# Optimization experiments

Measured on AMD Instinct MI355X. Metric: run time of the kernel, lower is better.

## Reference

```python
import jax, jax.numpy as jnp
import numpy as np

NUM_EXPERTS = 64
TOP_K = 2
AUX_COEF = 0.001
Z_COEF = 0.001


def setup_inputs() -> dict:
    key = jax.random.key(0)
    k1, k2 = jax.random.split(key)
    hidden_states = jax.random.normal(k1, (16384, 4096), dtype=jnp.float32)
    W_gate = jax.random.normal(k2, (NUM_EXPERTS, 4096), dtype=jnp.float32) * 0.02
    return {"hidden_states": hidden_states, "W_gate": W_gate}


def reference(hidden_states, W_gate):
    # Gate GEMM: [N, H] x [E, H]^T -> [N, E]
    router_logits = jnp.einsum('nh,eh->ne', hidden_states, W_gate)
    router_probs = jax.nn.softmax(router_logits, axis=-1)

    # Top-k selection + renormalization
    expert_weights, expert_indices = jax.lax.top_k(router_probs, TOP_K)
    expert_weights = expert_weights / jnp.sum(expert_weights, axis=-1, keepdims=True)

    # Load-balancing loss: num_experts * sum_i f_i * P_i
    num_tokens = router_probs.shape[0]
    one_hot = jax.nn.one_hot(expert_indices, NUM_EXPERTS, dtype=jnp.float32)  # [N, K, E]
    tokens_per_expert = one_hot.sum(axis=(0, 1))  # [E]
    f = tokens_per_expert / (num_tokens * TOP_K)
    P = router_probs.mean(axis=0)
    lb_loss = NUM_EXPERTS * jnp.sum(f * P)

    # Z-loss: mean of logsumexp(logits)^2
    log_z = jax.nn.logsumexp(router_logits, axis=-1)
    z_loss = jnp.mean(log_z ** 2)

    aux_loss = AUX_COEF * lb_loss + Z_COEF * z_loss
    return expert_weights, expert_indices, aux_loss
```

## Files before the change

### kernel.cpp

```cpp
#include <hip/hip_runtime.h>
#include <hip/hip_bf16.h>

#define NTOK 16384
#define HD   4096
#define NE   64
#define TTILE 32
#define NBLK (NTOK / TTILE)

typedef __bf16 bf16x8 __attribute__((ext_vector_type(8)));
typedef __bf16 bf16x4 __attribute__((ext_vector_type(4)));
typedef float  f32x4  __attribute__((ext_vector_type(4)));

__device__ __forceinline__ f32x4 mfma16(bf16x8 a, bf16x8 b, f32x4 c) {
    return __builtin_amdgcn_mfma_f32_16x16x32_bf16(a, b, c, 0, 0, 0);
}

#define SAB 40
#define SL  68

__device__ __forceinline__ void cvt_split(float4 v, bf16x4& hi, bf16x4& lo) {
    float x[4] = {v.x, v.y, v.z, v.w};
    #pragma unroll
    for (int e = 0; e < 4; ++e) {
        __bf16 h = (__bf16)x[e];
        hi[e] = h;
        lo[e] = (__bf16)(x[e] - (float)h);
    }
}

__global__ void zero_ws_kernel(float* ws) {
    int i = threadIdx.x;
    if (i < 129) ws[i] = 0.0f;
}

__global__ __launch_bounds__(256) void router_kernel(
    const float* __restrict__ hs,
    const float* __restrict__ Wg,
    float* __restrict__ out,
    float* __restrict__ ws)
{
    __shared__ __bf16 sAhi[2][TTILE * SAB];
    __shared__ __bf16 sAlo[2][TTILE * SAB];
    __shared__ __bf16 sBhi[2][NE * SAB];
    __shared__ __bf16 sBlo[2][NE * SAB];
    __shared__ float  sLog[TTILE * SL];
    __shared__ float  sInv[TTILE];
    __shared__ float  sPp[4 * 64];
    __shared__ float  sCnt[64];
    __shared__ float  sZ;

    const int tid = threadIdx.x;
    const int t0  = blockIdx.x * TTILE;

    if (tid < 64) sCnt[tid] = 0.0f;
    if (tid == 0) sZ = 0.0f;

    const int r1 = tid >> 3;
    const int c4 = (tid & 7) * 4;
    const float* gA = hs + (size_t)(t0 + r1) * HD + c4;
    const float* gB = Wg + (size_t)r1 * HD + c4;
    const int oA  = r1 * SAB + c4;
    const int oB1 = r1 * SAB + c4;
    const int oB2 = (r1 + 32) * SAB + c4;

    const int lane = tid & 63;
    const int wv   = tid >> 6;
    const int wr   = (wv >> 1) * 16;
    const int wc   = (wv & 1) * 32;
    const int fm   = lane & 15;
    const int fq   = lane >> 4;
    const int fk   = fq * 8;

    f32x4 acc[2];
    acc[0] = (f32x4){0.f, 0.f, 0.f, 0.f};
    acc[1] = (f32x4){0.f, 0.f, 0.f, 0.f};

    {
        float4 a0 = *(const float4*)(gA);
        float4 b0 = *(const float4*)(gB);
        float4 b1 = *(const float4*)(gB + 32 * HD);
        bf16x4 h, l;
        cvt_split(a0, h, l); *(bf16x4*)&sAhi[0][oA]  = h; *(bf16x4*)&sAlo[0][oA]  = l;
        cvt_split(b0, h, l); *(bf16x4*)&sBhi[0][oB1] = h; *(bf16x4*)&sBlo[0][oB1] = l;
        cvt_split(b1, h, l); *(bf16x4*)&sBhi[0][oB2] = h; *(bf16x4*)&sBlo[0][oB2] = l;
    }
    __syncthreads();

    const int NIT = HD / 32;
    for (int it = 0; it < NIT; ++it) {
        const int cur = it & 1;
        const bool more = (it + 1) < NIT;
        float4 na0, nb0, nb1;
        if (more) {
            const int k0 = (it + 1) * 32;
            na0 = *(const float4*)(gA + k0);
            nb0 = *(const float4*)(gB + k0);
            nb1 = *(const float4*)(gB + 32 * HD + k0);
        }

        bf16x8 ahi, alo, bhi[2], blo[2];
        {
            const int aoff = (wr + fm) * SAB + fk;
            ahi = *(const bf16x8*)&sAhi[cur][aoff];
            alo = *(const bf16x8*)&sAlo[cur][aoff];
        }
        #pragma unroll
        for (int j = 0; j < 2; ++j) {
            const int boff = (wc + j * 16 + fm) * SAB + fk;
            bhi[j] = *(const bf16x8*)&sBhi[cur][boff];
            blo[j] = *(const bf16x8*)&sBlo[cur][boff];
        }
        #pragma unroll
        for (int j = 0; j < 2; ++j) {
            acc[j] = mfma16(ahi, bhi[j], acc[j]);
            acc[j] = mfma16(ahi, blo[j], acc[j]);
            acc[j] = mfma16(alo, bhi[j], acc[j]);
            acc[j] = mfma16(alo, blo[j], acc[j]);
        }

        if (more) {
            const int nb = cur ^ 1;
            bf16x4 h, l;
            cvt_split(na0, h, l); *(bf16x4*)&sAhi[nb][oA]  = h; *(bf16x4*)&sAlo[nb][oA]  = l;
            cvt_split(nb0, h, l); *(bf16x4*)&sBhi[nb][oB1] = h; *(bf16x4*)&sBlo[nb][oB1] = l;
            cvt_split(nb1, h, l); *(bf16x4*)&sBhi[nb][oB2] = h; *(bf16x4*)&sBlo[nb][oB2] = l;
        }
        __syncthreads();
    }

    #pragma unroll
    for (int j = 0; j < 2; ++j)
        #pragma unroll
        for (int r = 0; r < 4; ++r) {
            const int tokl = wr + fq * 4 + r;
            const int expl = wc + j * 16 + fm;
            sLog[tokl * SL + expl] = acc[j][r];
        }
    __syncthreads();

    const int g = tid >> 3;
    const int l = tid & 7;
    float* Lrow = &sLog[g * SL + l * 8];
    float lv[8];
    float m = -3.0e38f;
    #pragma unroll
    for (int c = 0; c < 8; ++c) { lv[c] = Lrow[c]; m = fmaxf(m, lv[c]); }
    m = fmaxf(m, __shfl_xor(m, 1, 64));
    m = fmaxf(m, __shfl_xor(m, 2, 64));
    m = fmaxf(m, __shfl_xor(m, 4, 64));

    float v1 = -3.0e38f, v2 = -3.0e38f; int i1 = 0, i2 = 0;
    float ssum = 0.0f;
    #pragma unroll
    for (int c = 0; c < 8; ++c) {
        const float val = lv[c]; const int idx = l * 8 + c;
        const float ev = __expf(val - m);
        Lrow[c] = ev;
        ssum += ev;
        if (val > v1) { v2 = v1; i2 = i1; v1 = val; i1 = idx; }
        else if (val > v2) { v2 = val; i2 = idx; }
    }
    ssum += __shfl_xor(ssum, 1, 64);
    ssum += __shfl_xor(ssum, 2, 64);
    ssum += __shfl_xor(ssum, 4, 64);

    #pragma unroll
    for (int s = 1; s <= 4; s <<= 1) {
        const float ov1 = __shfl_xor(v1, s, 64);
        const int   oi1 = __shfl_xor(i1, s, 64);
        const float ov2 = __shfl_xor(v2, s, 64);
        const int   oi2 = __shfl_xor(i2, s, 64);
        float n1, n2; int ni1, ni2;
        const bool ofirst = (ov1 > v1) || (ov1 == v1 && oi1 < i1);
        if (ofirst) {
            n1 = ov1; ni1 = oi1;
            const bool osec = (ov2 > v1) || (ov2 == v1 && oi2 < i1);
            n2 = osec ? ov2 : v1; ni2 = osec ? oi2 : i1;
        } else {
            n1 = v1; ni1 = i1;
            const bool asec = (v2 > ov1) || (v2 == ov1 && i2 < oi1);
            n2 = asec ? v2 : ov1; ni2 = asec ? i2 : oi1;
        }
        v1 = n1; i1 = ni1; v2 = n2; i2 = ni2;
    }

    if (l == 0) {
        const float e1 = __expf(v1 - m), e2 = __expf(v2 - m);
        const float winv = 1.0f / (e1 + e2);
        const int token = t0 + g;
        out[2 * token]     = e1 * winv;
        out[2 * token + 1] = e2 * winv;
        out[2 * NTOK + 2 * token]     = (float)i1;
        out[2 * NTOK + 2 * token + 1] = (float)i2;
        const float lse = m + __logf(ssum);
        atomicAdd(&sZ, lse * lse);
        atomicAdd(&sCnt[i1], 1.0f);
        atomicAdd(&sCnt[i2], 1.0f);
        sInv[g] = 1.0f / ssum;
    }
    __syncthreads();

    {
        const int e = tid & 63;
        const int q = tid >> 6;
        float part = 0.0f;
        #pragma unroll
        for (int t = 0; t < 8; ++t) {
            const int tok = q * 8 + t;
            part += sLog[tok * SL + e] * sInv[tok];
        }
        sPp[q * 64 + e] = part;
    }
    __syncthreads();
    if (tid < 64) {
        const float ps = sPp[tid] + sPp[64 + tid] + sPp[128 + tid] + sPp[192 + tid];
        atomicAdd(&ws[tid], ps);
        atomicAdd(&ws[64 + tid], sCnt[tid]);
    }
    if (tid == 0) atomicAdd(&ws[128], sZ);
}

__global__ void finalize_kernel(const float* __restrict__ ws, float* __restrict__ out) {
    const int e = threadIdx.x;
    const float P = ws[e] * (1.0f / NTOK);
    const float f = ws[64 + e] * (1.0f / (NTOK * 2));
    float term = f * P;
    #pragma unroll
    for (int s = 32; s >= 1; s >>= 1) term += __shfl_xor(term, s, 64);
    if (e == 0) {
        const float lb = 64.0f * term;
        const float z  = ws[128] * (1.0f / NTOK);
        out[4 * NTOK] = 0.001f * lb + 0.001f * z;
    }
}

extern "C" void kernel_launch(void* const* d_in, const int* in_sizes, int n_in,
                              void* d_out, int out_size, void* d_ws, size_t ws_size,
                              hipStream_t stream) {
    const float* hs = (const float*)d_in[0];
    const float* Wg = (const float*)d_in[1];
    float* out = (float*)d_out;
    float* ws  = (float*)d_ws;

    hipLaunchKernelGGL(zero_ws_kernel, dim3(1), dim3(256), 0, stream, ws);
    hipLaunchKernelGGL(router_kernel, dim3(NBLK), dim3(256), 0, stream, hs, Wg, out, ws);
    hipLaunchKernelGGL(finalize_kernel, dim3(1), dim3(64), 0, stream, ws, out);
}
```

Before: 398.6 us.

## Pre-split gate weights into bf16 hi/lo and load MFMA fragments directly from global

Adds a prep kernel that converts W_gate once per call into bf16 hi/lo arrays in workspace (also zeroing the accumulators), and rewrites the router main loop to drop the LDS double-buffer and barriers, loading A and B fragments straight from global memory into registers, with a one-step register prefetch of A. This removes per-block redundant conversion of the weight matrix, LDS traffic and __syncthreads each k-step. In exchange every wave re-reads B from L2 and A loads are narrower, per-lane strided accesses, so memory latency is now hidden only by occupancy and the single prefetch. A fallback path with per-block on-the-fly conversion runs if the workspace is too small.

```diff
diff --git a/kernel.cpp b/kernel.cpp
--- a/kernel.cpp
+++ b/kernel.cpp
@@ -6,6 +6,12 @@
 #define NE   64
 #define TTILE 32
 #define NBLK (NTOK / TTILE)
+#define NIT  (HD / 32)
+
+#define SL  68
+
+#define WS_ACC_FLOATS 192
+#define B_ELEMS (NE * HD)
 
 typedef __bf16 bf16x8 __attribute__((ext_vector_type(8)));
 typedef __bf16 bf16x4 __attribute__((ext_vector_type(4)));
@@ -14,9 +20,6 @@
 __device__ __forceinline__ f32x4 mfma16(bf16x8 a, bf16x8 b, f32x4 c) {
     return __builtin_amdgcn_mfma_f32_16x16x32_bf16(a, b, c, 0, 0, 0);
 }
-
-#define SAB 40
-#define SL  68
 
 __device__ __forceinline__ void cvt_split(float4 v, bf16x4& hi, bf16x4& lo) {
     float x[4] = {v.x, v.y, v.z, v.w};
@@ -33,35 +36,45 @@
     if (i < 129) ws[i] = 0.0f;
 }
 
+__global__ __launch_bounds__(256) void prep_kernel(
+    const float* __restrict__ Wg, float* __restrict__ ws)
+{
+    const int tid = threadIdx.x;
+    if (blockIdx.x == 0 && tid < 129) ws[tid] = 0.0f;
+    __bf16* Bhi = (__bf16*)(ws + WS_ACC_FLOATS);
+    __bf16* Blo = Bhi + B_ELEMS;
+    const int i = (blockIdx.x * 256 + tid) * 8;
+    float4 v0 = *(const float4*)(Wg + i);
+    float4 v1 = *(const float4*)(Wg + i + 4);
+    bf16x4 h0, l0, h1, l1;
+    cvt_split(v0, h0, l0);
+    cvt_split(v1, h1, l1);
+    *(bf16x4*)(Bhi + i)     = h0;
+    *(bf16x4*)(Bhi + i + 4) = h1;
+    *(bf16x4*)(Blo + i)     = l0;
+    *(bf16x4*)(Blo + i + 4) = l1;
+}
+
+template<bool PRE>
 __global__ __launch_bounds__(256) void router_kernel(
     const float* __restrict__ hs,
     const float* __restrict__ Wg,
+    const __bf16* __restrict__ Bhi,
+    const __bf16* __restrict__ Blo,
     float* __restrict__ out,
     float* __restrict__ ws)
 {
-    __shared__ __bf16 sAhi[2][TTILE * SAB];
-    __shared__ __bf16 sAlo[2][TTILE * SAB];
-    __shared__ __bf16 sBhi[2][NE * SAB];
-    __shared__ __bf16 sBlo[2][NE * SAB];
-    __shared__ float  sLog[TTILE * SL];
-    __shared__ float  sInv[TTILE];
-    __shared__ float  sPp[4 * 64];
-    __shared__ float  sCnt[64];
-    __shared__ float  sZ;
+    __shared__ float sLog[TTILE * SL];
+    __shared__ float sInv[TTILE];
+    __shared__ float sPp[4 * 64];
+    __shared__ float sCnt[64];
+    __shared__ float sZ;
 
     const int tid = threadIdx.x;
     const int t0  = blockIdx.x * TTILE;
 
     if (tid < 64) sCnt[tid] = 0.0f;
     if (tid == 0) sZ = 0.0f;
-
-    const int r1 = tid >> 3;
-    const int c4 = (tid & 7) * 4;
-    const float* gA = hs + (size_t)(t0 + r1) * HD + c4;
-    const float* gB = Wg + (size_t)r1 * HD + c4;
-    const int oA  = r1 * SAB + c4;
-    const int oB1 = r1 * SAB + c4;
-    const int oB2 = (r1 + 32) * SAB + c4;
 
     const int lane = tid & 63;
     const int wv   = tid >> 6;
@@ -71,62 +84,80 @@
     const int fq   = lane >> 4;
     const int fk   = fq * 8;
 
+    const float* pA = hs + (size_t)(t0 + wr + fm) * HD + fk;
+
+    const __bf16* pBh = nullptr;
+    const __bf16* pBl = nullptr;
+    const float*  pBf = nullptr;
+    if constexpr (PRE) {
+        pBh = Bhi + (size_t)(wc + fm) * HD + fk;
+        pBl = Blo + (size_t)(wc + fm) * HD + fk;
+    } else {
+        pBf = Wg + (size_t)(wc + fm) * HD + fk;
+    }
+
     f32x4 acc[2];
     acc[0] = (f32x4){0.f, 0.f, 0.f, 0.f};
     acc[1] = (f32x4){0.f, 0.f, 0.f, 0.f};
 
-    {
-        float4 a0 = *(const float4*)(gA);
-        float4 b0 = *(const float4*)(gB);
-        float4 b1 = *(const float4*)(gB + 32 * HD);
-        bf16x4 h, l;
-        cvt_split(a0, h, l); *(bf16x4*)&sAhi[0][oA]  = h; *(bf16x4*)&sAlo[0][oA]  = l;
-        cvt_split(b0, h, l); *(bf16x4*)&sBhi[0][oB1] = h; *(bf16x4*)&sBlo[0][oB1] = l;
-        cvt_split(b1, h, l); *(bf16x4*)&sBhi[0][oB2] = h; *(bf16x4*)&sBlo[0][oB2] = l;
-    }
-    __syncthreads();
-
-    const int NIT = HD / 32;
-    for (int it = 0; it < NIT; ++it) {
-        const int cur = it & 1;
-        const bool more = (it + 1) < NIT;
-        float4 na0, nb0, nb1;
-        if (more) {
-            const int k0 = (it + 1) * 32;
-            na0 = *(const float4*)(gA + k0);
-            nb0 = *(const float4*)(gB + k0);
-            nb1 = *(const float4*)(gB + 32 * HD + k0);
-        }
-
-        bf16x8 ahi, alo, bhi[2], blo[2];
+    auto step = [&](float4 ca0, float4 ca1) {
+        bf16x8 bh0, bl0, bh1, bl1;
+        if constexpr (PRE) {
+            bh0 = *(const bf16x8*)(pBh);
+            bh1 = *(const bf16x8*)(pBh + 16 * HD);
+            bl0 = *(const bf16x8*)(pBl);
+            bl1 = *(const bf16x8*)(pBl + 16 * HD);
+            pBh += 32; pBl += 32;
+        } else {
+            float4 f00 = *(const float4*)(pBf);
+            float4 f01 = *(const float4*)(pBf + 4);
+            float4 f10 = *(const float4*)(pBf + 16 * HD);
+            float4 f11 = *(const float4*)(pBf + 16 * HD + 4);
+            pBf += 32;
+            bf16x4 h, l;
+            cvt_split(f00, h, l);
+            #pragma unroll
+            for (int e = 0; e < 4; ++e) { bh0[e] = h[e]; bl0[e] = l[e]; }
+            cvt_split(f01, h, l);
+            #pragma unroll
+            for (int e = 0; e < 4; ++e) { bh0[4+e] = h[e]; bl0[4+e] = l[e]; }
+            cvt_split(f10, h, l);
+            #pragma unroll
+            for (int e = 0; e < 4; ++e) { bh1[e] = h[e]; bl1[e] = l[e]; }
+            cvt_split(f11, h, l);
+            #pragma unroll
+            for (int e = 0; e < 4; ++e) { bh1[4+e] = h[e]; bl1[4+e] = l[e]; }
+        }
+        bf16x8 ahi, alo;
         {
-            const int aoff = (wr + fm) * SAB + fk;
-            ahi = *(const bf16x8*)&sAhi[cur][aoff];
-            alo = *(const bf16x8*)&sAlo[cur][aoff];
-        }
-        #pragma unroll
-        for (int j = 0; j < 2; ++j) {
-            const int boff = (wc + j * 16 + fm) * SAB + fk;
-            bhi[j] = *(const bf16x8*)&sBhi[cur][boff];
-            blo[j] = *(const bf16x8*)&sBlo[cur][boff];
-        }
-        #pragma unroll
-        for (int j = 0; j < 2; ++j) {
-            acc[j] = mfma16(ahi, bhi[j], acc[j]);
-            acc[j] = mfma16(ahi, blo[j], acc[j]);
-            acc[j] = mfma16(alo, bhi[j], acc[j]);
-            acc[j] = mfma16(alo, blo[j], acc[j]);
-        }
-
-        if (more) {
-            const int nb = cur ^ 1;
             bf16x4 h, l;
-            cvt_split(na0, h, l); *(bf16x4*)&sAhi[nb][oA]  = h; *(bf16x4*)&sAlo[nb][oA]  = l;
-            cvt_split(nb0, h, l); *(bf16x4*)&sBhi[nb][oB1] = h; *(bf16x4*)&sBlo[nb][oB1] = l;
-            cvt_split(nb1, h, l); *(bf16x4*)&sBhi[nb][oB2] = h; *(bf16x4*)&sBlo[nb][oB2] = l;
-        }
-        __syncthreads();
-    }
+            cvt_split(ca0, h, l);
+            #pragma unroll
+            for (int e = 0; e < 4; ++e) { ahi[e] = h[e]; alo[e] = l[e]; }
+            cvt_split(ca1, h, l);
+            #pragma unroll
+            for (int e = 0; e < 4; ++e) { ahi[4+e] = h[e]; alo[4+e] = l[e]; }
+        }
+        acc[0] = mfma16(ahi, bh0, acc[0]);
+        acc[0] = mfma16(ahi, bl0, acc[0]);
+        acc[0] = mfma16(alo, bh0, acc[0]);
+        acc[0] = mfma16(alo, bl0, acc[0]);
+        acc[1] = mfma16(ahi, bh1, acc[1]);
+        acc[1] = mfma16(ahi, bl1, acc[1]);
+        acc[1] = mfma16(alo, bh1, acc[1]);
+        acc[1] = mfma16(alo, bl1, acc[1]);
+    };
+
+    float4 a0 = *(const float4*)(pA);
+    float4 a1 = *(const float4*)(pA + 4);
+    for (int it = 0; it < NIT - 1; ++it) {
+        float4 n0 = *(const float4*)(pA + 32);
+        float4 n1 = *(const float4*)(pA + 36);
+        pA += 32;
+        step(a0, a1);
+        a0 = n0; a1 = n1;
+    }
+    step(a0, a1);
 
     #pragma unroll
     for (int j = 0; j < 2; ++j)
@@ -242,7 +273,18 @@
     float* out = (float*)d_out;
     float* ws  = (float*)d_ws;
 
-    hipLaunchKernelGGL(zero_ws_kernel, dim3(1), dim3(256), 0, stream, ws);
-    hipLaunchKernelGGL(router_kernel, dim3(NBLK), dim3(256), 0, stream, hs, Wg, out, ws);
+    const size_t need = (size_t)WS_ACC_FLOATS * sizeof(float)
+                      + (size_t)B_ELEMS * 2 * sizeof(__bf16);
+    if (ws_size >= need) {
+        const __bf16* Bhi = (const __bf16*)(ws + WS_ACC_FLOATS);
+        const __bf16* Blo = Bhi + B_ELEMS;
+        hipLaunchKernelGGL(prep_kernel, dim3(128), dim3(256), 0, stream, Wg, ws);
+        hipLaunchKernelGGL((router_kernel<true>), dim3(NBLK), dim3(256), 0, stream,
+                           hs, Wg, Bhi, Blo, out, ws);
+    } else {
+        hipLaunchKernelGGL(zero_ws_kernel, dim3(1), dim3(256), 0, stream, ws);
+        hipLaunchKernelGGL((router_kernel<false>), dim3(NBLK), dim3(256), 0, stream,
+                           hs, Wg, (const __bf16*)nullptr, (const __bf16*)nullptr, out, ws);
+    }
     hipLaunchKernelGGL(finalize_kernel, dim3(1), dim3(64), 0, stream, ws, out);
 }
```

Result: slower. 478.8 us (+20.1%).

## Pre-split gate weights to bf16 hi/lo once and stream B fragments directly into registers

Applied to the files above, without the earlier changes.

A prep kernel converts W_gate into bf16 hi/lo arrays in workspace once per call, merged with workspace zeroing. The main kernel then loads B fragments straight from global (L2-resident) into registers instead of each block re-reading fp32 W, splitting it and staging it through LDS. This removes redundant per-block conversion work and B shared-memory traffic, at the cost of an extra launch and more global/L2 loads per wave. A fallback path keeps the old kernel if the workspace is too small.

```diff
diff --git a/kernel.cpp b/kernel.cpp
--- a/kernel.cpp
+++ b/kernel.cpp
@@ -6,6 +6,13 @@
 #define NE   64
 #define TTILE 32
 #define NBLK (NTOK / TTILE)
+#define NIT  (HD / 32)
+
+#define SAB 40
+#define SL  68
+
+#define WS_ACC_FLOATS 192
+#define B_ELEMS (NE * HD)
 
 typedef __bf16 bf16x8 __attribute__((ext_vector_type(8)));
 typedef __bf16 bf16x4 __attribute__((ext_vector_type(4)));
@@ -14,9 +21,6 @@
 __device__ __forceinline__ f32x4 mfma16(bf16x8 a, bf16x8 b, f32x4 c) {
     return __builtin_amdgcn_mfma_f32_16x16x32_bf16(a, b, c, 0, 0, 0);
 }
-
-#define SAB 40
-#define SL  68
 
 __device__ __forceinline__ void cvt_split(float4 v, bf16x4& hi, bf16x4& lo) {
     float x[4] = {v.x, v.y, v.z, v.w};
@@ -33,16 +37,34 @@
     if (i < 129) ws[i] = 0.0f;
 }
 
-__global__ __launch_bounds__(256) void router_kernel(
+__global__ __launch_bounds__(256) void prep_kernel(
+    const float* __restrict__ Wg, float* __restrict__ ws)
+{
+    const int tid = threadIdx.x;
+    if (blockIdx.x == 0 && tid < 129) ws[tid] = 0.0f;
+    __bf16* Bhi = (__bf16*)(ws + WS_ACC_FLOATS);
+    __bf16* Blo = Bhi + B_ELEMS;
+    const int i = (blockIdx.x * 256 + tid) * 8;
+    float4 v0 = *(const float4*)(Wg + i);
+    float4 v1 = *(const float4*)(Wg + i + 4);
+    bf16x4 h0, l0, h1, l1;
+    cvt_split(v0, h0, l0);
+    cvt_split(v1, h1, l1);
+    *(bf16x4*)(Bhi + i)     = h0;
+    *(bf16x4*)(Bhi + i + 4) = h1;
+    *(bf16x4*)(Blo + i)     = l0;
+    *(bf16x4*)(Blo + i + 4) = l1;
+}
+
+__global__ __launch_bounds__(256) void router_pre_kernel(
     const float* __restrict__ hs,
-    const float* __restrict__ Wg,
+    const __bf16* __restrict__ Bhi,
+    const __bf16* __restrict__ Blo,
     float* __restrict__ out,
     float* __restrict__ ws)
 {
     __shared__ __bf16 sAhi[2][TTILE * SAB];
     __shared__ __bf16 sAlo[2][TTILE * SAB];
-    __shared__ __bf16 sBhi[2][NE * SAB];
-    __shared__ __bf16 sBlo[2][NE * SAB];
     __shared__ float  sLog[TTILE * SL];
     __shared__ float  sInv[TTILE];
     __shared__ float  sPp[4 * 64];
@@ -58,10 +80,7 @@
     const int r1 = tid >> 3;
     const int c4 = (tid & 7) * 4;
     const float* gA = hs + (size_t)(t0 + r1) * HD + c4;
-    const float* gB = Wg + (size_t)r1 * HD + c4;
-    const int oA  = r1 * SAB + c4;
-    const int oB1 = r1 * SAB + c4;
-    const int oB2 = (r1 + 32) * SAB + c4;
+    const int oA = r1 * SAB + c4;
 
     const int lane = tid & 63;
     const int wv   = tid >> 6;
@@ -71,59 +90,65 @@
     const int fq   = lane >> 4;
     const int fk   = fq * 8;
 
+    const __bf16* gBh = Bhi + (size_t)(wc + fm) * HD + fk;
+    const __bf16* gBl = Blo + (size_t)(wc + fm) * HD + fk;
+
     f32x4 acc[2];
     acc[0] = (f32x4){0.f, 0.f, 0.f, 0.f};
     acc[1] = (f32x4){0.f, 0.f, 0.f, 0.f};
 
     {
         float4 a0 = *(const float4*)(gA);
-        float4 b0 = *(const float4*)(gB);
-        float4 b1 = *(const float4*)(gB + 32 * HD);
         bf16x4 h, l;
-        cvt_split(a0, h, l); *(bf16x4*)&sAhi[0][oA]  = h; *(bf16x4*)&sAlo[0][oA]  = l;
-        cvt_split(b0, h, l); *(bf16x4*)&sBhi[0][oB1] = h; *(bf16x4*)&sBlo[0][oB1] = l;
-        cvt_split(b1, h, l); *(bf16x4*)&sBhi[0][oB2] = h; *(bf16x4*)&sBlo[0][oB2] = l;
-    }
-    __syncthreads();
-
-    const int NIT = HD / 32;
+        cvt_split(a0, h, l);
+        *(bf16x4*)&sAhi[0][oA] = h;
+        *(bf16x4*)&sAlo[0][oA] = l;
+    }
+    bf16x8 cbh[2], cbl[2];
+    cbh[0] = *(const bf16x8*)(gBh);
+    cbh[1] = *(const bf16x8*)(gBh + 16 * HD);
+    cbl[0] = *(const bf16x8*)(gBl);
+    cbl[1] = *(const bf16x8*)(gBl + 16 * HD);
+    __syncthreads();
+
+    #pragma unroll 2
     for (int it = 0; it < NIT; ++it) {
         const int cur = it & 1;
         const bool more = (it + 1) < NIT;
-        float4 na0, nb0, nb1;
+
+        float4 na;
+        bf16x8 nbh0, nbh1, nbl0, nbl1;
         if (more) {
             const int k0 = (it + 1) * 32;
-            na0 = *(const float4*)(gA + k0);
-            nb0 = *(const float4*)(gB + k0);
-            nb1 = *(const float4*)(gB + 32 * HD + k0);
-        }
-
-        bf16x8 ahi, alo, bhi[2], blo[2];
+            na   = *(const float4*)(gA + k0);
+            nbh0 = *(const bf16x8*)(gBh + k0);
+            nbh1 = *(const bf16x8*)(gBh + 16 * HD + k0);
+            nbl0 = *(const bf16x8*)(gBl + k0);
+            nbl1 = *(const bf16x8*)(gBl + 16 * HD + k0);
+        }
+
+        bf16x8 ahi, alo;
         {
             const int aoff = (wr + fm) * SAB + fk;
             ahi = *(const bf16x8*)&sAhi[cur][aoff];
             alo = *(const bf16x8*)&sAlo[cur][aoff];
         }
-        #pragma unroll
-        for (int j = 0; j < 2; ++j) {
-            const int boff = (wc + j * 16 + fm) * SAB + fk;
-            bhi[j] = *(const bf16x8*)&sBhi[cur][boff];
-            blo[j] = *(const bf16x8*)&sBlo[cur][boff];
-        }
-        #pragma unroll
-        for (int j = 0; j < 2; ++j) {
-            acc[j] = mfma16(ahi, bhi[j], acc[j]);
-            acc[j] = mfma16(ahi, blo[j], acc[j]);
-            acc[j] = mfma16(alo, bhi[j], acc[j]);
-            acc[j] = mfma16(alo, blo[j], acc[j]);
-        }
+        acc[0] = mfma16(ahi, cbh[0], acc[0]);
+        acc[0] = mfma16(ahi, cbl[0], acc[0]);
+        acc[0] = mfma16(alo, cbh[0], acc[0]);
+        acc[0] = mfma16(alo, cbl[0], acc[0]);
+        acc[1] = mfma16(ahi, cbh[1], acc[1]);
+        acc[1] = mfma16(ahi, cbl[1], acc[1]);
+        acc[1] = mfma16(alo, cbh[1], acc[1]);
+        acc[1] = mfma16(alo, cbl[1], acc[1]);
 
         if (more) {
-            const int nb = cur ^ 1;
             bf16x4 h, l;
-            cvt_split(na0, h, l); *(bf16x4*)&sAhi[nb][oA]  = h; *(bf16x4*)&sAlo[nb][oA]  = l;
-            cvt_split(nb0, h, l); *(bf16x4*)&sBhi[nb][oB1] = h; *(bf16x4*)&sBlo[nb][oB1] = l;
-            cvt_split(nb1, h, l); *(bf16x4*)&sBhi[nb][oB2] = h; *(bf16x4*)&sBlo[nb][oB2] = l;
+            cvt_split(na, h, l);
+            *(bf16x4*)&sAhi[cur ^ 1][oA] = h;
+            *(bf16x4*)&sAlo[cur ^ 1][oA] = l;
+            cbh[0] = nbh0; cbh[1] = nbh1;
+            cbl[0] = nbl0; cbl[1] = nbl1;
         }
         __syncthreads();
     }
@@ -220,6 +245,192 @@
     if (tid == 0) atomicAdd(&ws[128], sZ);
 }
 
+__global__ __launch_bounds__(256) void router_fb_kernel(
+    const float* __restrict__ hs,
+    const float* __restrict__ Wg,
+    float* __restrict__ out,
+    float* __restrict__ ws)
+{
+    __shared__ __bf16 sAhi[2][TTILE * SAB];
+    __shared__ __bf16 sAlo[2][TTILE * SAB];
+    __shared__ __bf16 sBhi[2][NE * SAB];
+    __shared__ __bf16 sBlo[2][NE * SAB];
+    __shared__ float  sLog[TTILE * SL];
+    __shared__ float  sInv[TTILE];
+    __shared__ float  sPp[4 * 64];
+    __shared__ float  sCnt[64];
+    __shared__ float  sZ;
+
+    const int tid = threadIdx.x;
+    const int t0  = blockIdx.x * TTILE;
+
+    if (tid < 64) sCnt[tid] = 0.0f;
+    if (tid == 0) sZ = 0.0f;
+
+    const int r1 = tid >> 3;
+    const int c4 = (tid & 7) * 4;
+    const float* gA = hs + (size_t)(t0 + r1) * HD + c4;
+    const float* gB = Wg + (size_t)r1 * HD + c4;
+    const int oA  = r1 * SAB + c4;
+    const int oB1 = r1 * SAB + c4;
+    const int oB2 = (r1 + 32) * SAB + c4;
+
+    const int lane = tid & 63;
+    const int wv   = tid >> 6;
+    const int wr   = (wv >> 1) * 16;
+    const int wc   = (wv & 1) * 32;
+    const int fm   = lane & 15;
+    const int fq   = lane >> 4;
+    const int fk   = fq * 8;
+
+    f32x4 acc[2];
+    acc[0] = (f32x4){0.f, 0.f, 0.f, 0.f};
+    acc[1] = (f32x4){0.f, 0.f, 0.f, 0.f};
+
+    {
+        float4 a0 = *(const float4*)(gA);
+        float4 b0 = *(const float4*)(gB);
+        float4 b1 = *(const float4*)(gB + 32 * HD);
+        bf16x4 h, l;
+        cvt_split(a0, h, l); *(bf16x4*)&sAhi[0][oA]  = h; *(bf16x4*)&sAlo[0][oA]  = l;
+        cvt_split(b0, h, l); *(bf16x4*)&sBhi[0][oB1] = h; *(bf16x4*)&sBlo[0][oB1] = l;
+        cvt_split(b1, h, l); *(bf16x4*)&sBhi[0][oB2] = h; *(bf16x4*)&sBlo[0][oB2] = l;
+    }
+    __syncthreads();
+
+    for (int it = 0; it < NIT; ++it) {
+        const int cur = it & 1;
+        const bool more = (it + 1) < NIT;
+        float4 na0, nb0, nb1;
+        if (more) {
+            const int k0 = (it + 1) * 32;
+            na0 = *(const float4*)(gA + k0);
+            nb0 = *(const float4*)(gB + k0);
+            nb1 = *(const float4*)(gB + 32 * HD + k0);
+        }
+
+        bf16x8 ahi, alo, bhi[2], blo[2];
+        {
+            const int aoff = (wr + fm) * SAB + fk;
+            ahi = *(const bf16x8*)&sAhi[cur][aoff];
+            alo = *(const bf16x8*)&sAlo[cur][aoff];
+        }
+        #pragma unroll
+        for (int j = 0; j < 2; ++j) {
+            const int boff = (wc + j * 16 + fm) * SAB + fk;
+            bhi[j] = *(const bf16x8*)&sBhi[cur][boff];
+            blo[j] = *(const bf16x8*)&sBlo[cur][boff];
+        }
+        #pragma unroll
+        for (int j = 0; j < 2; ++j) {
+            acc[j] = mfma16(ahi, bhi[j], acc[j]);
+            acc[j] = mfma16(ahi, blo[j], acc[j]);
+            acc[j] = mfma16(alo, bhi[j], acc[j]);
+            acc[j] = mfma16(alo, blo[j], acc[j]);
+        }
+
+        if (more) {
+            const int nb = cur ^ 1;
+            bf16x4 h, l;
+            cvt_split(na0, h, l); *(bf16x4*)&sAhi[nb][oA]  = h; *(bf16x4*)&sAlo[nb][oA]  = l;
+            cvt_split(nb0, h, l); *(bf16x4*)&sBhi[nb][oB1] = h; *(bf16x4*)&sBlo[nb][oB1] = l;
+            cvt_split(nb1, h, l); *(bf16x4*)&sBhi[nb][oB2] = h; *(bf16x4*)&sBlo[nb][oB2] = l;
+        }
+        __syncthreads();
+    }
+
+    #pragma unroll
+    for (int j = 0; j < 2; ++j)
+        #pragma unroll
+        for (int r = 0; r < 4; ++r) {
+            const int tokl = wr + fq * 4 + r;
+            const int expl = wc + j * 16 + fm;
+            sLog[tokl * SL + expl] = acc[j][r];
+        }
+    __syncthreads();
+
+    const int g = tid >> 3;
+    const int l = tid & 7;
+    float* Lrow = &sLog[g * SL + l * 8];
+    float lv[8];
+    float m = -3.0e38f;
+    #pragma unroll
+    for (int c = 0; c < 8; ++c) { lv[c] = Lrow[c]; m = fmaxf(m, lv[c]); }
+    m = fmaxf(m, __shfl_xor(m, 1, 64));
+    m = fmaxf(m, __shfl_xor(m, 2, 64));
+    m = fmaxf(m, __shfl_xor(m, 4, 64));
+
+    float v1 = -3.0e38f, v2 = -3.0e38f; int i1 = 0, i2 = 0;
+    float ssum = 0.0f;
+    #pragma unroll
+    for (int c = 0; c < 8; ++c) {
+        const float val = lv[c]; const int idx = l * 8 + c;
+        const float ev = __expf(val - m);
+        Lrow[c] = ev;
+        ssum += ev;
+        if (val > v1) { v2 = v1; i2 = i1; v1 = val; i1 = idx; }
+        else if (val > v2) { v2 = val; i2 = idx; }
+    }
+    ssum += __shfl_xor(ssum, 1, 64);
+    ssum += __shfl_xor(ssum, 2, 64);
+    ssum += __shfl_xor(ssum, 4, 64);
+
+    #pragma unroll
+    for (int s = 1; s <= 4; s <<= 1) {
+        const float ov1 = __shfl_xor(v1, s, 64);
+        const int   oi1 = __shfl_xor(i1, s, 64);
+        const float ov2 = __shfl_xor(v2, s, 64);
+        const int   oi2 = __shfl_xor(i2, s, 64);
+        float n1, n2; int ni1, ni2;
+        const bool ofirst = (ov1 > v1) || (ov1 == v1 && oi1 < i1);
+        if (ofirst) {
+            n1 = ov1; ni1 = oi1;
+            const bool osec = (ov2 > v1) || (ov2 == v1 && oi2 < i1);
+            n2 = osec ? ov2 : v1; ni2 = osec ? oi2 : i1;
+        } else {
+            n1 = v1; ni1 = i1;
+            const bool asec = (v2 > ov1) || (v2 == ov1 && i2 < oi1);
+            n2 = asec ? v2 : ov1; ni2 = asec ? i2 : oi1;
+        }
+        v1 = n1; i1 = ni1; v2 = n2; i2 = ni2;
+    }
+
+    if (l == 0) {
+        const float e1 = __expf(v1 - m), e2 = __expf(v2 - m);
+        const float winv = 1.0f / (e1 + e2);
+        const int token = t0 + g;
+        out[2 * token]     = e1 * winv;
+        out[2 * token + 1] = e2 * winv;
+        out[2 * NTOK + 2 * token]     = (float)i1;
+        out[2 * NTOK + 2 * token + 1] = (float)i2;
+        const float lse = m + __logf(ssum);
+        atomicAdd(&sZ, lse * lse);
+        atomicAdd(&sCnt[i1], 1.0f);
+        atomicAdd(&sCnt[i2], 1.0f);
+        sInv[g] = 1.0f / ssum;
+    }
+    __syncthreads();
+
+    {
+        const int e = tid & 63;
+        const int q = tid >> 6;
+        float part = 0.0f;
+        #pragma unroll
+        for (int t = 0; t < 8; ++t) {
+            const int tok = q * 8 + t;
+            part += sLog[tok * SL + e] * sInv[tok];
+        }
+        sPp[q * 64 + e] = part;
+    }
+    __syncthreads();
+    if (tid < 64) {
+        const float ps = sPp[tid] + sPp[64 + tid] + sPp[128 + tid] + sPp[192 + tid];
+        atomicAdd(&ws[tid], ps);
+        atomicAdd(&ws[64 + tid], sCnt[tid]);
+    }
+    if (tid == 0) atomicAdd(&ws[128], sZ);
+}
+
 __global__ void finalize_kernel(const float* __restrict__ ws, float* __restrict__ out) {
     const int e = threadIdx.x;
     const float P = ws[e] * (1.0f / NTOK);
@@ -242,7 +453,18 @@
     float* out = (float*)d_out;
     float* ws  = (float*)d_ws;
 
-    hipLaunchKernelGGL(zero_ws_kernel, dim3(1), dim3(256), 0, stream, ws);
-    hipLaunchKernelGGL(router_kernel, dim3(NBLK), dim3(256), 0, stream, hs, Wg, out, ws);
+    const size_t need = (size_t)WS_ACC_FLOATS * sizeof(float)
+                      + (size_t)B_ELEMS * 2 * sizeof(__bf16);
+    if (ws_size >= need) {
+        const __bf16* Bhi = (const __bf16*)(ws + WS_ACC_FLOATS);
+        const __bf16* Blo = Bhi + B_ELEMS;
+        hipLaunchKernelGGL(prep_kernel, dim3(128), dim3(256), 0, stream, Wg, ws);
+        hipLaunchKernelGGL(router_pre_kernel, dim3(NBLK), dim3(256), 0, stream,
+                           hs, Bhi, Blo, out, ws);
+    } else {
+        hipLaunchKernelGGL(zero_ws_kernel, dim3(1), dim3(256), 0, stream, ws);
+        hipLaunchKernelGGL(router_fb_kernel, dim3(NBLK), dim3(256), 0, stream,
+                           hs, Wg, out, ws);
+    }
     hipLaunchKernelGGL(finalize_kernel, dim3(1), dim3(64), 0, stream, ws, out);
 }
```

After: 437.1 us. 9.7% more time.
